# Optimization experiments

Measured on AMD Instinct MI355X. Metric: run time of the kernel, lower is better.

The kernel has to match this reference:

```python
import jax, jax.numpy as jnp
import numpy as np

B, S, P, D, H = 2, 4096, 1024, 1024, 16  # batch, byte seq, patches, d_model, heads


def setup_inputs() -> dict:
    key = jax.random.key(0)
    ks = jax.random.split(key, 8)
    init = 0.02
    queries = jax.random.normal(ks[0], (B, S, D), dtype=jnp.float32)
    patch_representations = jax.random.normal(ks[1], (B, P, D), dtype=jnp.float32)
    patch_boundaries = jax.random.randint(ks[2], (B, S), 0, 2, dtype=jnp.int32)
    wq = jax.random.normal(ks[3], (D, D), dtype=jnp.float32) * init
    wk = jax.random.normal(ks[4], (D, D), dtype=jnp.float32) * init
    wv = jax.random.normal(ks[5], (D, D), dtype=jnp.float32) * init
    wo = jax.random.normal(ks[6], (D, D), dtype=jnp.float32) * init
    bq = jnp.zeros((D,), jnp.float32)
    bk = jnp.zeros((D,), jnp.float32)
    bv = jnp.zeros((D,), jnp.float32)
    bo = jnp.zeros((D,), jnp.float32)
    return {"queries": queries, "patch_representations": patch_representations,
            "patch_boundaries": patch_boundaries,
            "wq": wq, "wk": wk, "wv": wv, "wo": wo,
            "bq": bq, "bk": bk, "bv": bv, "bo": bo}


def reference(queries, patch_representations, patch_boundaries,
              wq, wk, wv, wo, bq, bk, bv, bo):
    b, s, d = queries.shape
    p = patch_representations.shape[1]
    h = H
    dh = d // h
    scale = 1.0 / jnp.sqrt(jnp.asarray(dh, queries.dtype))

    # in-projections (torch Linear: x @ W.T + b)
    q = (queries @ wq.T + bq).reshape(b, s, h, dh)
    k = (patch_representations @ wk.T + bk).reshape(b, p, h, dh)
    v = (patch_representations @ wv.T + bv).reshape(b, p, h, dh)

    # scores: [b, h, s, p]
    scores = jnp.einsum('bqhd,bkhd->bhqk', q, k) * scale

    # data-dependent patch-boundary mask: byte t may attend to patch j iff j <= cumsum(boundaries)[t]
    patch_idx = jnp.cumsum(patch_boundaries, axis=1)          # [b, s]
    mask = jnp.arange(p)[None, None, :] > patch_idx[:, :, None]  # [b, s, p], True = masked
    scores = jnp.where(mask[:, None, :, :], jnp.finfo(scores.dtype).min, scores)

    attn = jax.nn.softmax(scores, axis=-1)                    # dropout inactive (eval)
    out = jnp.einsum('bhqk,bkhd->bqhd', attn, v).reshape(b, s, d)
    return out @ wo.T + bo
```

## Files before the change

kernel.cpp:

```cpp
#include <hip/hip_runtime.h>


#define B_ 2
#define S_ 4096
#define P_ 1024
#define D_ 1024
#define H_ 16
#define DH_ 64

#define NCONV 14336

typedef __attribute__((ext_vector_type(8))) short short8;
typedef __attribute__((ext_vector_type(4))) float f32x4;

#define KSCALE 0.18033688011112042f

#if __has_builtin(__builtin_amdgcn_exp2f)
#define EXP2(x) __builtin_amdgcn_exp2f(x)
#else
#define EXP2(x) exp2f(x)
#endif

static __device__ __forceinline__ unsigned short f2bf(float f) {
    unsigned int u = __float_as_uint(f);
    u += 0x7FFFu + ((u >> 16) & 1u);
    return (unsigned short)(u >> 16);
}

static __device__ __forceinline__ void gll16(const unsigned short* g,
                                             const unsigned short* l) {
    __builtin_amdgcn_global_load_lds(
        (const __attribute__((address_space(1))) unsigned int*)g,
        (__attribute__((address_space(3))) unsigned int*)l,
        16, 0, 0);
}

__global__ __launch_bounds__(256) void xattn_convert_all(
    const float* __restrict__ queries, const float* __restrict__ patches,
    const float* __restrict__ wq, const float* __restrict__ wk,
    const float* __restrict__ wv, const float* __restrict__ wo,
    unsigned short* __restrict__ qb, unsigned short* __restrict__ pb,
    unsigned short* __restrict__ wqb, unsigned short* __restrict__ wkb,
    unsigned short* __restrict__ wvb, unsigned short* __restrict__ wob,
    const int* __restrict__ bounds, int* __restrict__ pidx) {
    if (blockIdx.x >= NCONV) {
        __shared__ int sdata[256];
        int b = blockIdx.x - NCONV;
        int t = threadIdx.x;
        const int* src = bounds + b * S_ + t * 16;
        int vals[16];
        int run = 0;
#pragma unroll
        for (int i = 0; i < 16; ++i) { run += src[i]; vals[i] = run; }
        sdata[t] = run;
        __syncthreads();
        for (int off = 1; off < 256; off <<= 1) {
            int v = (t >= off) ? sdata[t - off] : 0;
            __syncthreads();
            sdata[t] += v;
            __syncthreads();
        }
        int prefix = (t > 0) ? sdata[t - 1] : 0;
        int* dst = pidx + b * S_ + t * 16;
#pragma unroll
        for (int i = 0; i < 16; ++i) dst[i] = prefix + vals[i];
        return;
    }
    const int NQ = (B_ * S_ * D_) / 4;
    const int NP = (B_ * P_ * D_) / 4;
    const int NW = (D_ * D_) / 4;
    int i = blockIdx.x * 256 + threadIdx.x;
    const float* src;
    unsigned short* dst;
    int j;
    if (i < NQ) { src = queries; dst = qb; j = i; }
    else if (i < NQ + NP) { src = patches; dst = pb; j = i - NQ; }
    else {
        int k = i - NQ - NP;
        int wsel = k >> 18;
        j = k & (NW - 1);
        if (wsel == 0) { src = wq; dst = wqb; }
        else if (wsel == 1) { src = wk; dst = wkb; }
        else if (wsel == 2) { src = wv; dst = wvb; }
        else { src = wo; dst = wob; }
    }
    float4 v = ((const float4*)src)[j];
    ushort4 o;
    o.x = f2bf(v.x); o.y = f2bf(v.y); o.z = f2bf(v.z); o.w = f2bf(v.w);
    ((ushort4*)dst)[j] = o;
}

__global__ __launch_bounds__(256) void xattn_gemm_qkv(
    const unsigned short* __restrict__ qb, const unsigned short* __restrict__ pb,
    const unsigned short* __restrict__ wqb, const unsigned short* __restrict__ wkb,
    const unsigned short* __restrict__ wvb,
    const float* __restrict__ bq, const float* __restrict__ bk,
    const float* __restrict__ bv,
    unsigned short* __restrict__ Qout, unsigned short* __restrict__ Kout,
    unsigned short* __restrict__ Vout) {
    const int K = 1024, N = 1024;
    const int z = blockIdx.z;
    if (z > 0 && blockIdx.y >= 16) return;
    const unsigned short* A = (z == 0) ? qb : pb;
    const unsigned short* W = (z == 0) ? wqb : ((z == 1) ? wkb : wvb);
    const float* bias = (z == 0) ? bq : ((z == 1) ? bk : bv);

    __shared__ unsigned short As[128 * 32];
    __shared__ unsigned short Bs[128 * 32];

    const int m0 = blockIdx.y * 128;
    const int n0 = blockIdx.x * 128;
    const int t = threadIdx.x;
    const int w = t >> 6;
    const int l = t & 63;
    const int fr = l & 15, fq = l >> 4;
    const int wr = w >> 1, wc = w & 1;

    const int r0s = t >> 2;
    const int cs = (t & 3) * 8;
    const unsigned short* Ap0 = A + (size_t)(m0 + r0s) * K + cs;
    const unsigned short* Ap1 = A + (size_t)(m0 + 64 + r0s) * K + cs;
    const unsigned short* Wp0 = W + (size_t)(n0 + r0s) * K + cs;
    const unsigned short* Wp1 = W + (size_t)(n0 + 64 + r0s) * K + cs;
    const unsigned short* lA0 = &As[(w * 64) * 8];
    const unsigned short* lA1 = &As[(256 + w * 64) * 8];
    const unsigned short* lB0 = &Bs[(w * 64) * 8];
    const unsigned short* lB1 = &Bs[(256 + w * 64) * 8];

    f32x4 acc[4][4];
#pragma unroll
    for (int i = 0; i < 4; ++i)
#pragma unroll
        for (int j = 0; j < 4; ++j) acc[i][j] = (f32x4){0.f, 0.f, 0.f, 0.f};

    for (int k0 = 0; k0 < K; k0 += 32) {
        gll16(Ap0 + k0, lA0);
        gll16(Ap1 + k0, lA1);
        gll16(Wp0 + k0, lB0);
        gll16(Wp1 + k0, lB1);
        __syncthreads();
        short8 af[4], bf[4];
#pragma unroll
        for (int i = 0; i < 4; ++i)
            af[i] = *(const short8*)&As[(wr * 64 + i * 16 + fr) * 32 + fq * 8];
#pragma unroll
        for (int j = 0; j < 4; ++j)
            bf[j] = *(const short8*)&Bs[(wc * 64 + j * 16 + fr) * 32 + fq * 8];
#pragma unroll
        for (int i = 0; i < 4; ++i)
#pragma unroll
            for (int j = 0; j < 4; ++j)
                acc[i][j] = __builtin_amdgcn_mfma_f32_16x16x32_bf16(af[i], bf[j], acc[i][j], 0, 0, 0);
        __syncthreads();
    }

#pragma unroll
    for (int j = 0; j < 4; ++j) {
        int n = n0 + wc * 64 + j * 16 + fr;
        float bvv = bias[n];
#pragma unroll
        for (int i = 0; i < 4; ++i) {
            int mbase = m0 + wr * 64 + i * 16 + fq * 4;
#pragma unroll
            for (int r = 0; r < 4; ++r) {
                float val = acc[i][j][r] + bvv;
                int m = mbase + r;
                if (z == 0) {
                    Qout[(size_t)m * N + n] = f2bf(val * KSCALE);
                } else if (z == 1) {
                    Kout[(size_t)m * N + n] = f2bf(val);
                } else {
                    int bb = m >> 10, c = m & (P_ - 1);
                    int hh = n >> 6, d = n & 63;
                    int cl = c & 63;
                    int cp = (c & 960) | (((cl & 15) << 2) | (cl >> 4));
                    Vout[(((size_t)(bb * H_ + hh)) * 64 + d) * P_ + cp] = f2bf(val);
                }
            }
        }
    }
}

__global__ __launch_bounds__(256) void xattn_gemm_o(
    const unsigned short* __restrict__ A,
    const unsigned short* __restrict__ W,
    const float* __restrict__ bias,
    float* __restrict__ Cout) {
    const int K = 1024, N = 1024;
    __shared__ unsigned short As[128 * 32];
    __shared__ unsigned short Bs[128 * 32];

    const int m0 = blockIdx.y * 128;
    const int n0 = blockIdx.x * 128;
    const int t = threadIdx.x;
    const int w = t >> 6;
    const int l = t & 63;
    const int fr = l & 15, fq = l >> 4;
    const int wr = w >> 1, wc = w & 1;

    const int r0s = t >> 2;
    const int cs = (t & 3) * 8;
    const unsigned short* Ap0 = A + (size_t)(m0 + r0s) * K + cs;
    const unsigned short* Ap1 = A + (size_t)(m0 + 64 + r0s) * K + cs;
    const unsigned short* Wp0 = W + (size_t)(n0 + r0s) * K + cs;
    const unsigned short* Wp1 = W + (size_t)(n0 + 64 + r0s) * K + cs;
    const unsigned short* lA0 = &As[(w * 64) * 8];
    const unsigned short* lA1 = &As[(256 + w * 64) * 8];
    const unsigned short* lB0 = &Bs[(w * 64) * 8];
    const unsigned short* lB1 = &Bs[(256 + w * 64) * 8];

    f32x4 acc[4][4];
#pragma unroll
    for (int i = 0; i < 4; ++i)
#pragma unroll
        for (int j = 0; j < 4; ++j) acc[i][j] = (f32x4){0.f, 0.f, 0.f, 0.f};

    for (int k0 = 0; k0 < K; k0 += 32) {
        gll16(Ap0 + k0, lA0);
        gll16(Ap1 + k0, lA1);
        gll16(Wp0 + k0, lB0);
        gll16(Wp1 + k0, lB1);
        __syncthreads();
        short8 af[4], bf[4];
#pragma unroll
        for (int i = 0; i < 4; ++i)
            af[i] = *(const short8*)&As[(wr * 64 + i * 16 + fr) * 32 + fq * 8];
#pragma unroll
        for (int j = 0; j < 4; ++j)
            bf[j] = *(const short8*)&Bs[(wc * 64 + j * 16 + fr) * 32 + fq * 8];
#pragma unroll
        for (int i = 0; i < 4; ++i)
#pragma unroll
            for (int j = 0; j < 4; ++j)
                acc[i][j] = __builtin_amdgcn_mfma_f32_16x16x32_bf16(af[i], bf[j], acc[i][j], 0, 0, 0);
        __syncthreads();
    }

#pragma unroll
    for (int j = 0; j < 4; ++j) {
        int n = n0 + wc * 64 + j * 16 + fr;
        float bvv = bias[n];
#pragma unroll
        for (int i = 0; i < 4; ++i) {
            int mbase = m0 + wr * 64 + i * 16 + fq * 4;
#pragma unroll
            for (int r = 0; r < 4; ++r)
                Cout[(size_t)(mbase + r) * N + n] = acc[i][j][r] + bvv;
        }
    }
}

__global__ __launch_bounds__(256) void xattn_attn_mfma(
    const unsigned short* __restrict__ Qb,
    const unsigned short* __restrict__ Kb,
    const unsigned short* __restrict__ Vtb,
    const int* __restrict__ pidx,
    unsigned short* __restrict__ Ob) {
    __shared__ unsigned short Ks[64 * 72];
    __shared__ unsigned short Vs[64 * 72];
    __shared__ unsigned short Ps[64 * 72];

    const int q0 = (63 - blockIdx.x) * 64;
    const int h = blockIdx.y;
    const int b = blockIdx.z;
    const int t = threadIdx.x;
    const int w = t >> 6, l = t & 63;
    const int fr = l & 15, fq = l >> 4;

    const unsigned short* qrow =
        Qb + (size_t)(b * S_ + q0 + w * 16 + fr) * D_ + h * DH_ + fq * 8;
    short8 qf0 = *(const short8*)qrow;
    short8 qf1 = *(const short8*)(qrow + 32);

    int prow[4];
#pragma unroll
    for (int r = 0; r < 4; ++r)
        prow[r] = pidx[b * S_ + q0 + w * 16 + fq * 4 + r];
    const int limit = pidx[b * S_ + q0 + 63];
    const int ntiles = (min(limit, P_ - 1) + 64) >> 6;
    const int nfull = (pidx[b * S_ + q0] + 1) >> 6;

    float lsum[4] = {0.f, 0.f, 0.f, 0.f};
    f32x4 oacc[4];
#pragma unroll
    for (int nt = 0; nt < 4; ++nt) oacc[nt] = (f32x4){0.f, 0.f, 0.f, 0.f};

    const int srow = t >> 3, sseg = t & 7;
    const unsigned short* kbase = Kb + (size_t)(b * P_) * D_ + h * DH_;
    const unsigned short* vbase = Vtb + (size_t)(b * H_ + h) * 64 * P_;

    for (int kt = 0; kt < ntiles; ++kt) {
        const int c0 = kt * 64;
        __syncthreads();
        *(uint4*)&Ks[srow * 72 + sseg * 8] =
            *(const uint4*)(kbase + (size_t)(c0 + srow) * D_ + sseg * 8);
        *(uint4*)&Ks[(srow + 32) * 72 + sseg * 8] =
            *(const uint4*)(kbase + (size_t)(c0 + srow + 32) * D_ + sseg * 8);
        *(uint4*)&Vs[srow * 72 + sseg * 8] =
            *(const uint4*)(vbase + (size_t)srow * P_ + c0 + sseg * 8);
        *(uint4*)&Vs[(srow + 32) * 72 + sseg * 8] =
            *(const uint4*)(vbase + (size_t)(srow + 32) * P_ + c0 + sseg * 8);
        __syncthreads();

        const int maskme = (kt >= nfull);
        f32x4 s[4];
#pragma unroll
        for (int nt = 0; nt < 4; ++nt) {
            short8 kf0 = *(const short8*)&Ks[(nt * 16 + fr) * 72 + fq * 8];
            short8 kf1 = *(const short8*)&Ks[(nt * 16 + fr) * 72 + 32 + fq * 8];
            f32x4 a = (f32x4){0.f, 0.f, 0.f, 0.f};
            a = __builtin_amdgcn_mfma_f32_16x16x32_bf16(qf0, kf0, a, 0, 0, 0);
            a = __builtin_amdgcn_mfma_f32_16x16x32_bf16(qf1, kf1, a, 0, 0, 0);
            s[nt] = a;
        }
        if (maskme) {
#pragma unroll
            for (int nt = 0; nt < 4; ++nt) {
                const int col = c0 + nt * 16 + fr;
#pragma unroll
                for (int r = 0; r < 4; ++r) {
                    float p = EXP2(s[nt][r]);
                    p = (col > prow[r]) ? 0.f : p;
                    s[nt][r] = p;
                    lsum[r] += p;
                }
            }
        } else {
#pragma unroll
            for (int nt = 0; nt < 4; ++nt) {
#pragma unroll
                for (int r = 0; r < 4; ++r) {
                    float p = EXP2(s[nt][r]);
                    s[nt][r] = p;
                    lsum[r] += p;
                }
            }
        }
#pragma unroll
        for (int r = 0; r < 4; ++r) {
            uint2 pk;
            pk.x = __builtin_amdgcn_perm(__float_as_uint(s[1][r]),
                                         __float_as_uint(s[0][r]), 0x07060302u);
            pk.y = __builtin_amdgcn_perm(__float_as_uint(s[3][r]),
                                         __float_as_uint(s[2][r]), 0x07060302u);
            *(uint2*)&Ps[(w * 16 + fq * 4 + r) * 72 + fr * 4] = pk;
        }
        short8 pf0 = *(const short8*)&Ps[(w * 16 + fr) * 72 + fq * 8];
        short8 pf1 = *(const short8*)&Ps[(w * 16 + fr) * 72 + 32 + fq * 8];
#pragma unroll
        for (int nt = 0; nt < 4; ++nt) {
            short8 vf0 = *(const short8*)&Vs[(nt * 16 + fr) * 72 + fq * 8];
            short8 vf1 = *(const short8*)&Vs[(nt * 16 + fr) * 72 + 32 + fq * 8];
            oacc[nt] = __builtin_amdgcn_mfma_f32_16x16x32_bf16(pf0, vf0, oacc[nt], 0, 0, 0);
            oacc[nt] = __builtin_amdgcn_mfma_f32_16x16x32_bf16(pf1, vf1, oacc[nt], 0, 0, 0);
        }
    }

#pragma unroll
    for (int off = 1; off < 16; off <<= 1) {
#pragma unroll
        for (int r = 0; r < 4; ++r)
            lsum[r] += __shfl_xor(lsum[r], off);
    }
    float inv[4];
#pragma unroll
    for (int r = 0; r < 4; ++r) inv[r] = 1.0f / lsum[r];

    unsigned short* obase = Ob + (size_t)(b * S_ + q0 + w * 16) * D_ + h * DH_;
#pragma unroll
    for (int nt = 0; nt < 4; ++nt)
#pragma unroll
        for (int r = 0; r < 4; ++r)
            obase[(size_t)(fq * 4 + r) * D_ + nt * 16 + fr] =
                f2bf(oacc[nt][r] * inv[r]);
}

extern "C" void kernel_launch(void* const* d_in, const int* in_sizes, int n_in,
                              void* d_out, int out_size, void* d_ws, size_t ws_size,
                              hipStream_t stream) {
    const float* queries = (const float*)d_in[0];
    const float* patches = (const float*)d_in[1];
    const int* bounds    = (const int*)d_in[2];
    const float* wq = (const float*)d_in[3];
    const float* wk = (const float*)d_in[4];
    const float* wv = (const float*)d_in[5];
    const float* wo = (const float*)d_in[6];
    const float* bq = (const float*)d_in[7];
    const float* bk = (const float*)d_in[8];
    const float* bv = (const float*)d_in[9];
    const float* bo = (const float*)d_in[10];
    float* out = (float*)d_out;

    char* ws = (char*)d_ws;
    unsigned short* qb    = (unsigned short*)(ws + 0);
    unsigned short* pb    = (unsigned short*)(ws + 16777216);
    unsigned short* wqb   = (unsigned short*)(ws + 20971520);
    unsigned short* wkb   = (unsigned short*)(ws + 23068672);
    unsigned short* wvb   = (unsigned short*)(ws + 25165824);
    unsigned short* wob   = (unsigned short*)(ws + 27262976);
    unsigned short* Qbf   = (unsigned short*)(ws + 29360128);
    unsigned short* Kbf   = (unsigned short*)(ws + 46137344);
    unsigned short* Vtb   = (unsigned short*)(ws + 50331648);
    unsigned short* attnb = (unsigned short*)(ws + 54525952);
    int* pidx             = (int*)(ws + 71303168);

    xattn_convert_all<<<dim3(NCONV + B_), 256, 0, stream>>>(
        queries, patches, wq, wk, wv, wo, qb, pb, wqb, wkb, wvb, wob,
        bounds, pidx);
    xattn_gemm_qkv<<<dim3(8, 64, 3), 256, 0, stream>>>(
        qb, pb, wqb, wkb, wvb, bq, bk, bv, Qbf, Kbf, Vtb);
    xattn_attn_mfma<<<dim3(S_ / 64, H_, B_), 256, 0, stream>>>(
        Qbf, Kbf, Vtb, pidx, attnb);
    xattn_gemm_o<<<dim3(8, 64), 256, 0, stream>>>(attnb, wob, bo, out);
}
```

Measured before the change: 245.5 us.

## Double-buffer K/V tiles with async global-to-LDS loads and XOR swizzle

```diff
diff --git a/kernel.cpp b/kernel.cpp
--- a/kernel.cpp
+++ b/kernel.cpp
@@ -99,8 +99,11 @@
     unsigned short* __restrict__ Qout, unsigned short* __restrict__ Kout,
     unsigned short* __restrict__ Vout) {
     const int K = 1024, N = 1024;
-    const int z = blockIdx.z;
-    if (z > 0 && blockIdx.y >= 16) return;
+    const int byy = blockIdx.y;
+    int z, my;
+    if (byy < 64)      { z = 0; my = byy; }
+    else if (byy < 80) { z = 1; my = byy - 64; }
+    else               { z = 2; my = byy - 80; }
     const unsigned short* A = (z == 0) ? qb : pb;
     const unsigned short* W = (z == 0) ? wqb : ((z == 1) ? wkb : wvb);
     const float* bias = (z == 0) ? bq : ((z == 1) ? bk : bv);
@@ -108,7 +111,7 @@
     __shared__ unsigned short As[128 * 32];
     __shared__ unsigned short Bs[128 * 32];
 
-    const int m0 = blockIdx.y * 128;
+    const int m0 = my * 128;
     const int n0 = blockIdx.x * 128;
     const int t = threadIdx.x;
     const int w = t >> 6;
@@ -256,9 +259,9 @@
     const unsigned short* __restrict__ Vtb,
     const int* __restrict__ pidx,
     unsigned short* __restrict__ Ob) {
-    __shared__ unsigned short Ks[64 * 72];
-    __shared__ unsigned short Vs[64 * 72];
-    __shared__ unsigned short Ps[64 * 72];
+    __shared__ unsigned short Ks[2][64 * 64];
+    __shared__ unsigned short Vs[2][64 * 64];
+    __shared__ unsigned short Ps[64 * 64];
 
     const int q0 = (63 - blockIdx.x) * 64;
     const int h = blockIdx.y;
@@ -285,34 +288,60 @@
 #pragma unroll
     for (int nt = 0; nt < 4; ++nt) oacc[nt] = (f32x4){0.f, 0.f, 0.f, 0.f};
 
-    const int srow = t >> 3, sseg = t & 7;
+    const int srow = l >> 3;
+    const int g = (l & 7) ^ srow;
     const unsigned short* kbase = Kb + (size_t)(b * P_) * D_ + h * DH_;
     const unsigned short* vbase = Vtb + (size_t)(b * H_ + h) * 64 * P_;
+    const unsigned short* kp0 = kbase + (size_t)(w * 16 + srow) * D_ + g * 8;
+    const unsigned short* kp1 = kp0 + (size_t)8 * D_;
+    const unsigned short* vp0 = vbase + (size_t)(w * 16 + srow) * P_ + g * 8;
+    const unsigned short* vp1 = vp0 + (size_t)8 * P_;
+
+    gll16(kp0, &Ks[0][w * 1024]);
+    gll16(kp1, &Ks[0][w * 1024 + 512]);
+    gll16(vp0, &Vs[0][w * 1024]);
+    gll16(vp1, &Vs[0][w * 1024 + 512]);
+    kp0 += (size_t)64 * D_; kp1 += (size_t)64 * D_;
+    vp0 += 64; vp1 += 64;
+
+    const int sw = (fq ^ (fr & 7)) * 8;
+    int cur = 0;
 
     for (int kt = 0; kt < ntiles; ++kt) {
+        __builtin_amdgcn_s_barrier();
+        if (kt + 1 < ntiles) {
+            const int nb = cur ^ 1;
+            gll16(kp0, &Ks[nb][w * 1024]);
+            gll16(kp1, &Ks[nb][w * 1024 + 512]);
+            gll16(vp0, &Vs[nb][w * 1024]);
+            gll16(vp1, &Vs[nb][w * 1024 + 512]);
+            kp0 += (size_t)64 * D_; kp1 += (size_t)64 * D_;
+            vp0 += 64; vp1 += 64;
+            asm volatile("s_waitcnt vmcnt(4)" ::: "memory");
+        } else {
+            asm volatile("s_waitcnt vmcnt(0)" ::: "memory");
+        }
+        __builtin_amdgcn_sched_barrier(0);
+        __builtin_amdgcn_s_barrier();
+
+        const unsigned short* Kc = Ks[cur];
+        const unsigned short* Vc = Vs[cur];
         const int c0 = kt * 64;
-        __syncthreads();
-        *(uint4*)&Ks[srow * 72 + sseg * 8] =
-            *(const uint4*)(kbase + (size_t)(c0 + srow) * D_ + sseg * 8);
-        *(uint4*)&Ks[(srow + 32) * 72 + sseg * 8] =
-            *(const uint4*)(kbase + (size_t)(c0 + srow + 32) * D_ + sseg * 8);
-        *(uint4*)&Vs[srow * 72 + sseg * 8] =
-            *(const uint4*)(vbase + (size_t)srow * P_ + c0 + sseg * 8);
-        *(uint4*)&Vs[(srow + 32) * 72 + sseg * 8] =
-            *(const uint4*)(vbase + (size_t)(srow + 32) * P_ + c0 + sseg * 8);
-        __syncthreads();
-
         const int maskme = (kt >= nfull);
+
         f32x4 s[4];
+        __builtin_amdgcn_s_setprio(1);
 #pragma unroll
         for (int nt = 0; nt < 4; ++nt) {
-            short8 kf0 = *(const short8*)&Ks[(nt * 16 + fr) * 72 + fq * 8];
-            short8 kf1 = *(const short8*)&Ks[(nt * 16 + fr) * 72 + 32 + fq * 8];
+            short8 kf0 = *(const short8*)&Kc[(nt * 16 + fr) * 64 + sw];
+            short8 kf1 = *(const short8*)&Kc[(nt * 16 + fr) * 64 + (sw ^ 32)];
             f32x4 a = (f32x4){0.f, 0.f, 0.f, 0.f};
             a = __builtin_amdgcn_mfma_f32_16x16x32_bf16(qf0, kf0, a, 0, 0, 0);
             a = __builtin_amdgcn_mfma_f32_16x16x32_bf16(qf1, kf1, a, 0, 0, 0);
             s[nt] = a;
         }
+        __builtin_amdgcn_s_setprio(0);
+
         if (maskme) {
 #pragma unroll
             for (int nt = 0; nt < 4; ++nt) {
@@ -336,6 +365,7 @@
                 }
             }
         }
+
 #pragma unroll
         for (int r = 0; r < 4; ++r) {
             uint2 pk;
@@ -343,17 +373,25 @@
                                          __float_as_uint(s[0][r]), 0x07060302u);
             pk.y = __builtin_amdgcn_perm(__float_as_uint(s[3][r]),
                                          __float_as_uint(s[2][r]), 0x07060302u);
-            *(uint2*)&Ps[(w * 16 + fq * 4 + r) * 72 + fr * 4] = pk;
-        }
-        short8 pf0 = *(const short8*)&Ps[(w * 16 + fr) * 72 + fq * 8];
-        short8 pf1 = *(const short8*)&Ps[(w * 16 + fr) * 72 + 32 + fq * 8];
+            const int pr = w * 16 + fq * 4 + r;
+            const int pg = (((fr >> 1) ^ (pr & 7)) << 3) | ((fr & 1) << 2);
+            *(uint2*)&Ps[pr * 64 + pg] = pk;
+        }
+
+        const int prr = (w * 16 + fr) * 64;
+        short8 pf0 = *(const short8*)&Ps[prr + sw];
+        short8 pf1 = *(const short8*)&Ps[prr + (sw ^ 32)];
+        __builtin_amdgcn_s_setprio(1);
 #pragma unroll
         for (int nt = 0; nt < 4; ++nt) {
-            short8 vf0 = *(const short8*)&Vs[(nt * 16 + fr) * 72 + fq * 8];
-            short8 vf1 = *(const short8*)&Vs[(nt * 16 + fr) * 72 + 32 + fq * 8];
+            short8 vf0 = *(const short8*)&Vc[(nt * 16 + fr) * 64 + sw];
+            short8 vf1 = *(const short8*)&Vc[(nt * 16 + fr) * 64 + (sw ^ 32)];
             oacc[nt] = __builtin_amdgcn_mfma_f32_16x16x32_bf16(pf0, vf0, oacc[nt], 0, 0, 0);
             oacc[nt] = __builtin_amdgcn_mfma_f32_16x16x32_bf16(pf1, vf1, oacc[nt], 0, 0, 0);
         }
+        __builtin_amdgcn_s_setprio(0);
+
+        cur ^= 1;
     }
 
 #pragma unroll
@@ -407,7 +445,7 @@
     xattn_convert_all<<<dim3(NCONV + B_), 256, 0, stream>>>(
         queries, patches, wq, wk, wv, wo, qb, pb, wqb, wkb, wvb, wob,
         bounds, pidx);
-    xattn_gemm_qkv<<<dim3(8, 64, 3), 256, 0, stream>>>(
+    xattn_gemm_qkv<<<dim3(8, 96), 256, 0, stream>>>(
         qb, pb, wqb, wkb, wvb, bq, bk, bv, Qbf, Kbf, Vtb);
     xattn_attn_mfma<<<dim3(S_ / 64, H_, B_), 256, 0, stream>>>(
         Qbf, Kbf, Vtb, pidx, attnb);
```

Result: faster. 236.1 us (-3.8%).
